# Performance work log

Measured on AMD Instinct MI355X. Metric: run time of the kernel, lower is better.

The kernel has to match this reference:

```python
import jax, jax.numpy as jnp
import numpy as np

HEADS = 12
LN_EPS = 1e-5


def setup_inputs() -> dict:
    B, S, D = 2, 2048, 768
    k = jax.random.key(0)
    ks = jax.random.split(k, 16)
    std = 0.02
    inp = {
        "key": jax.random.normal(ks[0], (B, S, D), jnp.float32),
        "query": jax.random.normal(ks[1], (B, S, D), jnp.float32),
        "value": jax.random.normal(ks[2], (B, S, D), jnp.float32),
        "mask": jax.random.randint(ks[3], (B, S, S), 0, 2).astype(bool),
        "Wk_w": jax.random.normal(ks[4], (D, D), jnp.float32) * std,
        "Wk_b": jnp.zeros((D,), jnp.float32),
        "Wq_w": jax.random.normal(ks[5], (D, D), jnp.float32) * std,
        "Wq_b": jnp.zeros((D,), jnp.float32),
        "Wv_w": jax.random.normal(ks[6], (D, D), jnp.float32) * std,
        "Wv_b": jnp.zeros((D,), jnp.float32),
        "Wc_w": jax.random.normal(ks[7], (D, D), jnp.float32) * std,
        "Wc_b": jnp.zeros((D,), jnp.float32),
        "ln_g": jnp.ones((D,), jnp.float32),
        "ln_b": jnp.zeros((D,), jnp.float32),
    }
    return inp


def _mha(key, query, value, mask, Wk_w, Wk_b, Wq_w, Wq_b, Wv_w, Wv_b,
         Wc_w, Wc_b, ln_g, ln_b):
    B, Sq, D = query.shape
    Sk = key.shape[1]
    H = HEADS
    hd = D // H
    scaler = np.float32(D ** 0.5)  # NOTE: source scales by sqrt(hidden_size), not sqrt(head_dim)

    # QKV projections (torch Linear: x @ W.T + b)
    hk = (key @ Wk_w.T + Wk_b).reshape(B, Sk, H, hd).transpose(2, 0, 1, 3)    # (H,B,Sk,hd)
    hq = (query @ Wq_w.T + Wq_b).reshape(B, Sq, H, hd).transpose(2, 0, 1, 3)  # (H,B,Sq,hd)
    hv = (value @ Wv_w.T + Wv_b).reshape(B, Sk, H, hd).transpose(2, 0, 1, 3)  # (H,B,Sk,hd)

    qk = jnp.einsum('hbqd,hbkd->hbqk', hq, hk) / scaler
    qk = jnp.where(mask[None], -jnp.inf, qk)  # mask repeated over heads in source
    attn = jax.nn.softmax(qk, axis=-1)        # dropout is identity in eval
    out = jnp.einsum('hbqk,hbkd->hbqd', attn, hv)  # (H,B,Sq,hd)

    # Faithful replication of source reshape chain:
    # (H*B,Sq,hd).view(B,H,Sq,hd).permute(1,2,0,3).view(B,Sq,D)
    out = out.reshape(B, H, Sq, hd)             # flat reinterpretation, head-major data
    out = jnp.transpose(out, (1, 2, 0, 3)).reshape(B, Sq, D)

    out = out @ Wc_w.T + Wc_b                   # Wconcat; dropout identity
    x = out + query                             # residual
    mu = jnp.mean(x, axis=-1, keepdims=True)
    var = jnp.mean((x - mu) ** 2, axis=-1, keepdims=True)
    return ln_g * (x - mu) / jnp.sqrt(var + LN_EPS) + ln_b


def reference(key, query, value, mask, Wk_w, Wk_b, Wq_w, Wq_b, Wv_w, Wv_b,
              Wc_w, Wc_b, ln_g, ln_b):
    return _mha(key, query, value, mask, Wk_w, Wk_b, Wq_w, Wq_b,
                Wv_w, Wv_b, Wc_w, Wc_b, ln_g, ln_b)
```

## Files before the change

kernel.cpp:

```cpp
#include <hip/hip_runtime.h>
#include <stdint.h>

typedef float v4f __attribute__((ext_vector_type(4)));
typedef short v8s __attribute__((ext_vector_type(8)));

#define AS1 __attribute__((address_space(1)))
#define AS3 __attribute__((address_space(3)))

__device__ __forceinline__ void load16_to_lds(const void* g, void* l) {
  __builtin_amdgcn_global_load_lds((AS1 void*)g, (AS3 void*)l, 16, 0, 0);
}
__device__ __forceinline__ void load4_to_lds(const void* g, void* l) {
  __builtin_amdgcn_global_load_lds((AS1 void*)g, (AS3 void*)l, 4, 0, 0);
}

__device__ __forceinline__ float fexp2(float x) {
#if __has_builtin(__builtin_amdgcn_exp2f)
  return __builtin_amdgcn_exp2f(x);
#else
  return exp2f(x);
#endif
}

__device__ __forceinline__ unsigned short f2bf_rn(float f) {
  union { float f; uint32_t u; } v; v.f = f;
  return (unsigned short)((v.u + 0x8000u) >> 16);
}
__device__ __forceinline__ uint32_t pack_bf2(float x, float y) {
  union { float f; uint32_t u; } a, b; a.f = x; b.f = y;
  return __builtin_amdgcn_perm(b.u + 0x8000u, a.u + 0x8000u, 0x07060302u);
}

#define QSCALE 0.052058786f

__global__ __launch_bounds__(256) void pack_mask_kernel(
    const uint32_t* __restrict__ mask, uint32_t* __restrict__ bits) {
  __shared__ int s_i32;
  const int tid = threadIdx.x;
  if (tid == 0) s_i32 = 1;
  __syncthreads();
  if (mask[tid] > 1u) s_i32 = 0;
  __syncthreads();
  if (s_i32) {
    const int lane = tid & 63;
    const int gw = (blockIdx.x * 256 + tid) >> 6;
#pragma unroll 4
    for (int it = 0; it < 32; ++it) {
      const size_t base = (size_t)gw * 2048 + it * 64;
      unsigned long long bal = __ballot(mask[base + lane] != 0u);
      if (lane == 0) *(unsigned long long*)&bits[base >> 5] = bal;
    }
  } else {
    const int wi = blockIdx.x * 256 + tid;
    const uint32_t* p = mask + (size_t)wi * 8;
    uint32_t w = 0;
#pragma unroll
    for (int j8 = 0; j8 < 8; ++j8) {
      uint32_t u = p[j8];
#pragma unroll
      for (int k = 0; k < 4; ++k)
        w |= (((u >> (8 * k)) & 0xFFu) ? 1u : 0u) << (j8 * 4 + k);
    }
    bits[wi] = w;
  }
}

__global__ __launch_bounds__(256) void conv_kernel(
    const float* __restrict__ wk, const float* __restrict__ wq,
    const float* __restrict__ wv, const float* __restrict__ wc,
    const float* __restrict__ kin, const float* __restrict__ qin,
    const float* __restrict__ vin,
    unsigned short* __restrict__ dk, unsigned short* __restrict__ dq,
    unsigned short* __restrict__ dv, unsigned short* __restrict__ dc,
    unsigned short* __restrict__ dki, unsigned short* __restrict__ dqi,
    unsigned short* __restrict__ dvi) {
  const int y = blockIdx.y;
  const float* s; unsigned short* d; float sc = 1.f; int n4;
  switch (y) {
    case 0: s = wk;  d = dk;  n4 = 147456; break;
    case 1: s = wq;  d = dq;  n4 = 147456; sc = QSCALE; break;
    case 2: s = wv;  d = dv;  n4 = 147456; break;
    case 3: s = wc;  d = dc;  n4 = 147456; break;
    case 4: s = kin; d = dki; n4 = 786432; break;
    case 5: s = qin; d = dqi; n4 = 786432; break;
    default: s = vin; d = dvi; n4 = 786432; break;
  }
  const int i = blockIdx.x * 256 + threadIdx.x;
  if (i >= n4) return;
  float4 f = ((const float4*)s)[i];
  uint2 o;
  o.x = pack_bf2(f.x * sc, f.y * sc);
  o.y = pack_bf2(f.z * sc, f.w * sc);
  ((uint2*)d)[i] = o;
}

__global__ __launch_bounds__(256, 3) void gemm_qkv_kernel(
    const unsigned short* __restrict__ qin, const unsigned short* __restrict__ kin,
    const unsigned short* __restrict__ vin,
    const unsigned short* __restrict__ wqb, const unsigned short* __restrict__ wkb,
    const unsigned short* __restrict__ wvb,
    const float* __restrict__ bq, const float* __restrict__ bk,
    const float* __restrict__ bv,
    unsigned short* __restrict__ Qb, unsigned short* __restrict__ Kb,
    unsigned short* __restrict__ Vt) {
  const int which = blockIdx.z;
  const unsigned short* A; const unsigned short* Wb; const float* bias;
  float bscale = 1.f;
  if (which == 0)      { A = qin; Wb = wqb; bias = bq; bscale = QSCALE; }
  else if (which == 1) { A = kin; Wb = wkb; bias = bk; }
  else                 { A = vin; Wb = wvb; bias = bv; }

  const int m0 = blockIdx.x * 128, n0 = blockIdx.y * 128;
  const int tid = threadIdx.x, lane = tid & 63, wid = tid >> 6;
  const int wm = wid >> 1, wn = wid & 1;
  const int l16 = lane & 15, quad = lane >> 4;

  __shared__ __align__(16) unsigned short As[2][128 * 32];
  __shared__ __align__(16) unsigned short Bs[2][128 * 32];

  v4f acc[4][4];
#pragma unroll
  for (int i = 0; i < 4; ++i)
#pragma unroll
    for (int j = 0; j < 4; ++j) { v4f z = {0.f, 0.f, 0.f, 0.f}; acc[i][j] = z; }

  const int c0 = wid * 128 + lane, c1 = wid * 128 + 64 + lane;
  const unsigned short* a0 = A + (size_t)(m0 + (c0 >> 2)) * 768 + (c0 & 3) * 8;
  const unsigned short* a1 = A + (size_t)(m0 + (c1 >> 2)) * 768 + (c1 & 3) * 8;
  const unsigned short* b0 = Wb + (size_t)(n0 + (c0 >> 2)) * 768 + (c0 & 3) * 8;
  const unsigned short* b1 = Wb + (size_t)(n0 + (c1 >> 2)) * 768 + (c1 & 3) * 8;

#define QKV_STAGE(k0, buf)                                         \
  do {                                                             \
    load16_to_lds(a0 + (k0), &As[buf][(wid * 128) * 8]);           \
    load16_to_lds(a1 + (k0), &As[buf][(wid * 128 + 64) * 8]);      \
    load16_to_lds(b0 + (k0), &Bs[buf][(wid * 128) * 8]);           \
    load16_to_lds(b1 + (k0), &Bs[buf][(wid * 128 + 64) * 8]);      \
  } while (0)

  QKV_STAGE(0, 0);
#pragma unroll 2
  for (int ks = 0; ks < 24; ++ks) {
    const int bufc = ks & 1;
    __syncthreads();
    v8s af[4], bf[4];
#pragma unroll
    for (int i = 0; i < 4; ++i)
      af[i] = *(const v8s*)&As[bufc][(wm * 64 + i * 16 + l16) * 32 + quad * 8];
#pragma unroll
    for (int j = 0; j < 4; ++j)
      bf[j] = *(const v8s*)&Bs[bufc][(wn * 64 + j * 16 + l16) * 32 + quad * 8];
    if (ks < 23) QKV_STAGE((ks + 1) * 32, bufc ^ 1);
#pragma unroll
    for (int i = 0; i < 4; ++i)
#pragma unroll
      for (int j = 0; j < 4; ++j)
        acc[i][j] = __builtin_amdgcn_mfma_f32_16x16x32_bf16(af[i], bf[j],
                                                            acc[i][j], 0, 0, 0);
  }
#undef QKV_STAGE

#pragma unroll
  for (int i = 0; i < 4; ++i) {
#pragma unroll
    for (int j = 0; j < 4; ++j) {
      const int mbase = m0 + wm * 64 + i * 16 + quad * 4;
      const int n = n0 + wn * 64 + j * 16 + l16;
      const float bv_ = bias[n] * bscale;
      if (which == 2) {
        const int bb = mbase >> 11, ss = mbase & 2047;
        uint2 pk;
        pk.x = pack_bf2(acc[i][j][0] + bv_, acc[i][j][1] + bv_);
        pk.y = pack_bf2(acc[i][j][2] + bv_, acc[i][j][3] + bv_);
        *(uint2*)&Vt[((size_t)bb * 768 + n) * 2048 + ss] = pk;
      } else {
        unsigned short* dst = (which == 0) ? Qb : Kb;
#pragma unroll
        for (int r = 0; r < 4; ++r)
          dst[(size_t)(mbase + r) * 768 + n] = f2bf_rn(acc[i][j][r] + bv_);
      }
    }
  }
}

__global__ __launch_bounds__(256, 3) void attn_kernel(
    const unsigned short* __restrict__ Qb, const unsigned short* __restrict__ Kb,
    const unsigned short* __restrict__ Vt, const uint32_t* __restrict__ mbits,
    unsigned short* __restrict__ X) {
  const int q0 = blockIdx.x * 64;
  const int h = blockIdx.y, b = blockIdx.z;
  const int tid = threadIdx.x, w = tid >> 6, lane = tid & 63;
  const int l16 = lane & 15, quad = lane >> 4, l7 = l16 & 7;

  __shared__ __align__(16) unsigned short Kl[2][64 * 64];
  __shared__ __align__(16) unsigned short Vl[2][64 * 64];
  __shared__ __align__(16) unsigned short Pl[4][16 * 64];
  __shared__ uint32_t Ml[2][128];

  v8s aq[2];
  {
    const unsigned short* qp =
        Qb + (size_t)(b * 2048 + q0 + w * 16 + l16) * 768 + h * 64 + quad * 8;
    aq[0] = *(const v8s*)qp;
    aq[1] = *(const v8s*)(qp + 32);
  }

  v4f o[4], ol;
#pragma unroll
  for (int nt = 0; nt < 4; ++nt) { v4f z = {0.f, 0.f, 0.f, 0.f}; o[nt] = z; }
  { v4f z = {0.f, 0.f, 0.f, 0.f}; ol = z; }

  v8s bones;
  {
    const short v1 = (l16 == 0) ? (short)0x3F80 : (short)0;
#pragma unroll
    for (int j = 0; j < 8; ++j) bones[j] = v1;
  }

  const int rsub = lane >> 3;
  const int csub = ((lane & 7) ^ rsub) * 8;
  const unsigned short* kg0 = Kb + (size_t)(b * 2048 + w * 16) * 768 + h * 64;
  const unsigned short* vg0 = Vt + (size_t)(b * 768 + h * 64 + w * 16) * 2048;
  const uint32_t* mg0 =
      mbits + (size_t)(b * 2048 + q0 + w * 32 + (lane >> 1)) * 64 + (lane & 1);

#define ATTN_STAGE(kk0, buf)                                                  \
  do {                                                                        \
    const unsigned short* kg = kg0 + (size_t)(kk0) * 768;                     \
    const unsigned short* vg = vg0 + (kk0);                                   \
    load16_to_lds(kg + (size_t)rsub * 768 + csub, &Kl[buf][(w * 16) * 64]);   \
    load16_to_lds(kg + (size_t)(8 + rsub) * 768 + csub,                       \
                  &Kl[buf][(w * 16 + 8) * 64]);                               \
    load16_to_lds(vg + (size_t)rsub * 2048 + csub, &Vl[buf][(w * 16) * 64]);  \
    load16_to_lds(vg + (size_t)(8 + rsub) * 2048 + csub,                      \
                  &Vl[buf][(w * 16 + 8) * 64]);                               \
    if (w < 2) load4_to_lds(mg0 + ((kk0) >> 5), &Ml[buf][w * 64]);            \
  } while (0)

  ATTN_STAGE(0, 0);
#pragma unroll 2
  for (int it = 0; it < 32; ++it) {
    const int bufc = it & 1;
    __syncthreads();

    v8s bk[2][4];
#pragma unroll
    for (int kt = 0; kt < 2; ++kt)
#pragma unroll
      for (int nt = 0; nt < 4; ++nt)
        bk[kt][nt] = *(const v8s*)&Kl[bufc][(nt * 16 + l16) * 64 +
                                           (((kt * 4 + quad) ^ l7) << 3)];
    if (it < 31) ATTN_STAGE((it + 1) * 64, bufc ^ 1);

    v4f sacc[4];
#pragma unroll
    for (int nt = 0; nt < 4; ++nt) { v4f z = {0.f, 0.f, 0.f, 0.f}; sacc[nt] = z; }
#pragma unroll
    for (int kt = 0; kt < 2; ++kt)
#pragma unroll
      for (int nt = 0; nt < 4; ++nt)
        sacc[nt] = __builtin_amdgcn_mfma_f32_16x16x32_bf16(aq[kt], bk[kt][nt],
                                                           sacc[nt], 0, 0, 0);

    const int rowb = w * 16 + quad * 4;
    const int hi = l16 >> 3;
#pragma unroll
    for (int r = 0; r < 4; ++r) {
      const uint2 mw = *(const uint2*)&Ml[bufc][(rowb + r - w * 16 + w * 16) * 2];
      const uint32_t u0 = mw.x >> l16, u1 = mw.y >> l16;
      const float p0 = (u0 & 1u) ? 0.f : fexp2(sacc[0][r]);
      const float p1 = ((u0 >> 16) & 1u) ? 0.f : fexp2(sacc[1][r]);
      const float p2 = (u1 & 1u) ? 0.f : fexp2(sacc[2][r]);
      const float p3 = ((u1 >> 16) & 1u) ? 0.f : fexp2(sacc[3][r]);
      const int prow = quad * 4 + r, ps = prow & 7;
      const int base = prow * 64 + l7;
      Pl[w][base + (((0 + hi) ^ ps) << 3)] = f2bf_rn(p0);
      Pl[w][base + (((2 + hi) ^ ps) << 3)] = f2bf_rn(p1);
      Pl[w][base + (((4 + hi) ^ ps) << 3)] = f2bf_rn(p2);
      Pl[w][base + (((6 + hi) ^ ps) << 3)] = f2bf_rn(p3);
    }

#pragma unroll
    for (int kt = 0; kt < 2; ++kt) {
      const v8s ap = *(const v8s*)&Pl[w][l16 * 64 + (((kt * 4 + quad) ^ l7) << 3)];
#pragma unroll
      for (int nt = 0; nt < 4; ++nt) {
        const v8s bv = *(const v8s*)&Vl[bufc][(nt * 16 + l16) * 64 +
                                             (((kt * 4 + quad) ^ l7) << 3)];
        o[nt] = __builtin_amdgcn_mfma_f32_16x16x32_bf16(ap, bv, o[nt], 0, 0, 0);
      }
      ol = __builtin_amdgcn_mfma_f32_16x16x32_bf16(ap, bones, ol, 0, 0, 0);
    }
  }
#undef ATTN_STAGE

  const int hb2 = 2 * h + b;
  const int b2 = (hb2 >= 12) ? 1 : 0;
  const int h2 = hb2 - 12 * b2;
#pragma unroll
  for (int r = 0; r < 4; ++r) {
    const float lsum = __shfl(ol[r], quad * 16, 64);
    const float inv_l = 1.f / lsum;
    const int q = q0 + w * 16 + quad * 4 + r;
#pragma unroll
    for (int nt = 0; nt < 4; ++nt) {
      const int d = nt * 16 + l16;
      const size_t f = (size_t)h2 * 262144 + (size_t)q * 128 + b2 * 64 + d;
      X[f] = f2bf_rn(o[nt][r] * inv_l);
    }
  }
}

__global__ __launch_bounds__(256, 3) void gemm2_kernel(
    const unsigned short* __restrict__ X, const unsigned short* __restrict__ Wcb,
    const float* __restrict__ bc, const float* __restrict__ query,
    float* __restrict__ out) {
  const int m0 = blockIdx.x * 64, n0 = blockIdx.y * 128;
  const int tid = threadIdx.x, lane = tid & 63, wid = tid >> 6;
  const int wm = wid >> 1, wn = wid & 1;
  const int l16 = lane & 15, quad = lane >> 4;

  __shared__ __align__(16) unsigned short As[2][64 * 32];
  __shared__ __align__(16) unsigned short Bs[2][128 * 32];

  v4f acc[2][4];
#pragma unroll
  for (int i = 0; i < 2; ++i)
#pragma unroll
    for (int j = 0; j < 4; ++j) { v4f z = {0.f, 0.f, 0.f, 0.f}; acc[i][j] = z; }

  const int ca = tid;
  const unsigned short* a0 = X + (size_t)(m0 + (ca >> 2)) * 768 + (ca & 3) * 8;
  const int c0 = wid * 128 + lane, c1 = wid * 128 + 64 + lane;
  const unsigned short* b0 = Wcb + (size_t)(n0 + (c0 >> 2)) * 768 + (c0 & 3) * 8;
  const unsigned short* b1 = Wcb + (size_t)(n0 + (c1 >> 2)) * 768 + (c1 & 3) * 8;

#define G2_STAGE(k0, buf)                                        \
  do {                                                           \
    load16_to_lds(a0 + (k0), &As[buf][(wid * 64) * 8]);          \
    load16_to_lds(b0 + (k0), &Bs[buf][(wid * 128) * 8]);         \
    load16_to_lds(b1 + (k0), &Bs[buf][(wid * 128 + 64) * 8]);    \
  } while (0)

  G2_STAGE(0, 0);
#pragma unroll 2
  for (int ks = 0; ks < 24; ++ks) {
    const int bufc = ks & 1;
    __syncthreads();
    v8s af[2], bf[4];
#pragma unroll
    for (int i = 0; i < 2; ++i)
      af[i] = *(const v8s*)&As[bufc][(wm * 32 + i * 16 + l16) * 32 + quad * 8];
#pragma unroll
    for (int j = 0; j < 4; ++j)
      bf[j] = *(const v8s*)&Bs[bufc][(wn * 64 + j * 16 + l16) * 32 + quad * 8];
    if (ks < 23) G2_STAGE((ks + 1) * 32, bufc ^ 1);
#pragma unroll
    for (int i = 0; i < 2; ++i)
#pragma unroll
      for (int j = 0; j < 4; ++j)
        acc[i][j] = __builtin_amdgcn_mfma_f32_16x16x32_bf16(af[i], bf[j],
                                                            acc[i][j], 0, 0, 0);
  }
#undef G2_STAGE

#pragma unroll
  for (int i = 0; i < 2; ++i) {
#pragma unroll
    for (int j = 0; j < 4; ++j) {
      const int mbase = m0 + wm * 32 + i * 16 + quad * 4;
      const int n = n0 + wn * 64 + j * 16 + l16;
      const float bv_ = bc[n];
#pragma unroll
      for (int r = 0; r < 4; ++r) {
        const int m = mbase + r;
        out[(size_t)m * 768 + n] =
            acc[i][j][r] + bv_ + query[(size_t)m * 768 + n];
      }
    }
  }
}

__global__ __launch_bounds__(256) void ln_kernel(float* __restrict__ out,
                                                 const float* __restrict__ g,
                                                 const float* __restrict__ bta) {
  const int row = blockIdx.x;
  const int tid = threadIdx.x;
  float x[3];
  float s = 0.f, sq = 0.f;
#pragma unroll
  for (int k = 0; k < 3; ++k) {
    x[k] = out[(size_t)row * 768 + tid + k * 256];
    s += x[k];
    sq += x[k] * x[k];
  }
#pragma unroll
  for (int off = 1; off < 64; off <<= 1) {
    s += __shfl_xor(s, off, 64);
    sq += __shfl_xor(sq, off, 64);
  }
  __shared__ float ss[4], ssq[4];
  const int w = tid >> 6, lane = tid & 63;
  if (lane == 0) { ss[w] = s; ssq[w] = sq; }
  __syncthreads();
  s = ss[0] + ss[1] + ss[2] + ss[3];
  sq = ssq[0] + ssq[1] + ssq[2] + ssq[3];
  const float mu = s * (1.f / 768.f);
  const float var = sq * (1.f / 768.f) - mu * mu;
  const float rstd = rsqrtf(var + 1e-5f);
#pragma unroll
  for (int k = 0; k < 3; ++k) {
    const int cc = tid + k * 256;
    out[(size_t)row * 768 + cc] = g[cc] * (x[k] - mu) * rstd + bta[cc];
  }
}

extern "C" void kernel_launch(void* const* d_in, const int* in_sizes, int n_in,
                              void* d_out, int out_size, void* d_ws,
                              size_t ws_size, hipStream_t stream) {
  const float* key   = (const float*)d_in[0];
  const float* query = (const float*)d_in[1];
  const float* value = (const float*)d_in[2];
  const uint32_t* mask = (const uint32_t*)d_in[3];
  const float* Wk = (const float*)d_in[4];
  const float* bk = (const float*)d_in[5];
  const float* Wq = (const float*)d_in[6];
  const float* bq = (const float*)d_in[7];
  const float* Wv = (const float*)d_in[8];
  const float* bv = (const float*)d_in[9];
  const float* Wc = (const float*)d_in[10];
  const float* bc = (const float*)d_in[11];
  const float* lng = (const float*)d_in[12];
  const float* lnb = (const float*)d_in[13];

  char* ws = (char*)d_ws;
  uint32_t*       mbits = (uint32_t*)(ws);
  unsigned short* Wkb = (unsigned short*)(ws + 0x100000);
  unsigned short* Wqb = (unsigned short*)(ws + 0x220000);
  unsigned short* Wvb = (unsigned short*)(ws + 0x340000);
  unsigned short* Wcb = (unsigned short*)(ws + 0x460000);
  unsigned short* Qb  = (unsigned short*)(ws + 0x600000);
  unsigned short* Kb  = (unsigned short*)(ws + 0xC00000);
  unsigned short* Vt  = (unsigned short*)(ws + 0x1200000);
  unsigned short* X   = (unsigned short*)(ws + 0x1800000);
  unsigned short* Kin = (unsigned short*)d_out;
  unsigned short* Qin = (unsigned short*)d_out + 3145728;
  unsigned short* Vin = X;
  float* out = (float*)d_out;

  pack_mask_kernel<<<dim3(1024), dim3(256), 0, stream>>>(mask, mbits);
  conv_kernel<<<dim3(3072, 7), dim3(256), 0, stream>>>(
      Wk, Wq, Wv, Wc, key, query, value,
      Wkb, Wqb, Wvb, Wcb, Kin, Qin, Vin);
  gemm_qkv_kernel<<<dim3(32, 6, 3), dim3(256), 0, stream>>>(
      Qin, Kin, Vin, Wqb, Wkb, Wvb, bq, bk, bv, Qb, Kb, Vt);
  attn_kernel<<<dim3(32, 12, 2), dim3(256), 0, stream>>>(Qb, Kb, Vt, mbits, X);
  gemm2_kernel<<<dim3(64, 6), dim3(256), 0, stream>>>(X, Wcb, bc, query, out);
  ln_kernel<<<dim3(4096), dim3(256), 0, stream>>>(out, lng, lnb);
}
```

Before: 243.9 us.

## Fuse mask packing into conversion, split attention keys across waves, fuse GEMM2 with LayerNorm

Result: slower. 264.1 us (+8.3%).

```diff
diff --git a/kernel.cpp b/kernel.cpp
--- a/kernel.cpp
+++ b/kernel.cpp
@@ -33,48 +33,48 @@
 
 #define QSCALE 0.052058786f
 
-__global__ __launch_bounds__(256) void pack_mask_kernel(
-    const uint32_t* __restrict__ mask, uint32_t* __restrict__ bits) {
-  __shared__ int s_i32;
-  const int tid = threadIdx.x;
-  if (tid == 0) s_i32 = 1;
-  __syncthreads();
-  if (mask[tid] > 1u) s_i32 = 0;
-  __syncthreads();
-  if (s_i32) {
-    const int lane = tid & 63;
-    const int gw = (blockIdx.x * 256 + tid) >> 6;
-#pragma unroll 4
-    for (int it = 0; it < 32; ++it) {
-      const size_t base = (size_t)gw * 2048 + it * 64;
-      unsigned long long bal = __ballot(mask[base + lane] != 0u);
-      if (lane == 0) *(unsigned long long*)&bits[base >> 5] = bal;
-    }
-  } else {
-    const int wi = blockIdx.x * 256 + tid;
-    const uint32_t* p = mask + (size_t)wi * 8;
-    uint32_t w = 0;
-#pragma unroll
-    for (int j8 = 0; j8 < 8; ++j8) {
-      uint32_t u = p[j8];
-#pragma unroll
-      for (int k = 0; k < 4; ++k)
-        w |= (((u >> (8 * k)) & 0xFFu) ? 1u : 0u) << (j8 * 4 + k);
-    }
-    bits[wi] = w;
-  }
-}
-
-__global__ __launch_bounds__(256) void conv_kernel(
+__global__ __launch_bounds__(256) void conv_pack_kernel(
     const float* __restrict__ wk, const float* __restrict__ wq,
     const float* __restrict__ wv, const float* __restrict__ wc,
     const float* __restrict__ kin, const float* __restrict__ qin,
-    const float* __restrict__ vin,
+    const float* __restrict__ vin, const uint32_t* __restrict__ mask,
     unsigned short* __restrict__ dk, unsigned short* __restrict__ dq,
     unsigned short* __restrict__ dv, unsigned short* __restrict__ dc,
     unsigned short* __restrict__ dki, unsigned short* __restrict__ dqi,
-    unsigned short* __restrict__ dvi) {
+    unsigned short* __restrict__ dvi, uint32_t* __restrict__ bits) {
   const int y = blockIdx.y;
+  const int tid = threadIdx.x;
+  if (y == 7) {
+    if (blockIdx.x >= 1024) return;
+    __shared__ int s_i32;
+    if (tid == 0) s_i32 = 1;
+    __syncthreads();
+    if (mask[tid] > 1u) s_i32 = 0;
+    __syncthreads();
+    if (s_i32) {
+      const int lane = tid & 63;
+      const int gw = (blockIdx.x * 256 + tid) >> 6;
+#pragma unroll 4
+      for (int it = 0; it < 32; ++it) {
+        const size_t base = (size_t)gw * 2048 + it * 64;
+        unsigned long long bal = __ballot(mask[base + lane] != 0u);
+        if (lane == 0) *(unsigned long long*)&bits[base >> 5] = bal;
+      }
+    } else {
+      const int wi = blockIdx.x * 256 + tid;
+      const uint32_t* p = mask + (size_t)wi * 8;
+      uint32_t w = 0;
+#pragma unroll
+      for (int j8 = 0; j8 < 8; ++j8) {
+        uint32_t u = p[j8];
+#pragma unroll
+        for (int k = 0; k < 4; ++k)
+          w |= (((u >> (8 * k)) & 0xFFu) ? 1u : 0u) << (j8 * 4 + k);
+      }
+      bits[wi] = w;
+    }
+    return;
+  }
   const float* s; unsigned short* d; float sc = 1.f; int n4;
   switch (y) {
     case 0: s = wk;  d = dk;  n4 = 147456; break;
@@ -85,7 +85,7 @@
     case 5: s = qin; d = dqi; n4 = 786432; break;
     default: s = vin; d = dvi; n4 = 786432; break;
   }
-  const int i = blockIdx.x * 256 + threadIdx.x;
+  const int i = blockIdx.x * 256 + tid;
   if (i >= n4) return;
   float4 f = ((const float4*)s)[i];
   uint2 o;
@@ -191,24 +191,32 @@
   const int h = blockIdx.y, b = blockIdx.z;
   const int tid = threadIdx.x, w = tid >> 6, lane = tid & 63;
   const int l16 = lane & 15, quad = lane >> 4, l7 = l16 & 7;
-
-  __shared__ __align__(16) unsigned short Kl[2][64 * 64];
-  __shared__ __align__(16) unsigned short Vl[2][64 * 64];
-  __shared__ __align__(16) unsigned short Pl[4][16 * 64];
-  __shared__ uint32_t Ml[2][128];
-
-  v8s aq[2];
-  {
+  const int wq = w >> 1, wk = w & 1;
+
+  __shared__ __align__(16) char smem[41984];
+  unsigned short* Kl = (unsigned short*)smem;
+  unsigned short* Vl = (unsigned short*)(smem + 16384);
+  unsigned short* Pl = (unsigned short*)(smem + 32768);
+  uint32_t*       Ml = (uint32_t*)(smem + 40960);
+  float*          sc = (float*)smem;
+
+  v8s aq[2][2];
+#pragma unroll
+  for (int mi = 0; mi < 2; ++mi) {
     const unsigned short* qp =
-        Qb + (size_t)(b * 2048 + q0 + w * 16 + l16) * 768 + h * 64 + quad * 8;
-    aq[0] = *(const v8s*)qp;
-    aq[1] = *(const v8s*)(qp + 32);
-  }
-
-  v4f o[4], ol;
-#pragma unroll
-  for (int nt = 0; nt < 4; ++nt) { v4f z = {0.f, 0.f, 0.f, 0.f}; o[nt] = z; }
-  { v4f z = {0.f, 0.f, 0.f, 0.f}; ol = z; }
+        Qb + (size_t)(b * 2048 + q0 + wq * 32 + mi * 16 + l16) * 768 + h * 64 +
+        quad * 8;
+    aq[mi][0] = *(const v8s*)qp;
+    aq[mi][1] = *(const v8s*)(qp + 32);
+  }
+
+  v4f o[2][4], ol[2];
+#pragma unroll
+  for (int mi = 0; mi < 2; ++mi) {
+#pragma unroll
+    for (int nt = 0; nt < 4; ++nt) { v4f z = {0.f, 0.f, 0.f, 0.f}; o[mi][nt] = z; }
+    v4f z = {0.f, 0.f, 0.f, 0.f}; ol[mi] = z;
+  }
 
   v8s bones;
   {
@@ -224,17 +232,19 @@
   const uint32_t* mg0 =
       mbits + (size_t)(b * 2048 + q0 + w * 32 + (lane >> 1)) * 64 + (lane & 1);
 
-#define ATTN_STAGE(kk0, buf)                                                  \
-  do {                                                                        \
-    const unsigned short* kg = kg0 + (size_t)(kk0) * 768;                     \
-    const unsigned short* vg = vg0 + (kk0);                                   \
-    load16_to_lds(kg + (size_t)rsub * 768 + csub, &Kl[buf][(w * 16) * 64]);   \
-    load16_to_lds(kg + (size_t)(8 + rsub) * 768 + csub,                       \
-                  &Kl[buf][(w * 16 + 8) * 64]);                               \
-    load16_to_lds(vg + (size_t)rsub * 2048 + csub, &Vl[buf][(w * 16) * 64]);  \
-    load16_to_lds(vg + (size_t)(8 + rsub) * 2048 + csub,                      \
-                  &Vl[buf][(w * 16 + 8) * 64]);                               \
-    if (w < 2) load4_to_lds(mg0 + ((kk0) >> 5), &Ml[buf][w * 64]);            \
+#define ATTN_STAGE(kk0, buf)                                                   \
+  do {                                                                         \
+    const unsigned short* kg = kg0 + (size_t)(kk0) * 768;                      \
+    const unsigned short* vg = vg0 + (kk0);                                    \
+    load16_to_lds(kg + (size_t)rsub * 768 + csub,                              \
+                  &Kl[(buf) * 4096 + (w * 16) * 64]);                          \
+    load16_to_lds(kg + (size_t)(8 + rsub) * 768 + csub,                        \
+                  &Kl[(buf) * 4096 + (w * 16 + 8) * 64]);                      \
+    load16_to_lds(vg + (size_t)rsub * 2048 + csub,                             \
+                  &Vl[(buf) * 4096 + (w * 16) * 64]);                          \
+    load16_to_lds(vg + (size_t)(8 + rsub) * 2048 + csub,                       \
+                  &Vl[(buf) * 4096 + (w * 16 + 8) * 64]);                      \
+    if (w < 2) load4_to_lds(mg0 + ((kk0) >> 5), &Ml[(buf) * 128 + w * 64]);    \
   } while (0)
 
   ATTN_STAGE(0, 0);
@@ -243,103 +253,135 @@
     const int bufc = it & 1;
     __syncthreads();
 
-    v8s bk[2][4];
+    v8s bk[2][2];
+#pragma unroll
+    for (int ni = 0; ni < 2; ++ni)
+#pragma unroll
+      for (int kt = 0; kt < 2; ++kt)
+        bk[ni][kt] = *(const v8s*)&Kl[bufc * 4096 +
+                                      (wk * 32 + ni * 16 + l16) * 64 +
+                                      (((kt * 4 + quad) ^ l7) << 3)];
+    if (it < 31) ATTN_STAGE((it + 1) * 64, bufc ^ 1);
+
+    v4f sacc[2][2];
+#pragma unroll
+    for (int mi = 0; mi < 2; ++mi)
+#pragma unroll
+      for (int ni = 0; ni < 2; ++ni) {
+        v4f z = {0.f, 0.f, 0.f, 0.f};
+        sacc[mi][ni] = z;
+      }
 #pragma unroll
     for (int kt = 0; kt < 2; ++kt)
 #pragma unroll
+      for (int mi = 0; mi < 2; ++mi)
+#pragma unroll
+        for (int ni = 0; ni < 2; ++ni)
+          sacc[mi][ni] = __builtin_amdgcn_mfma_f32_16x16x32_bf16(
+              aq[mi][kt], bk[ni][kt], sacc[mi][ni], 0, 0, 0);
+
+    const int hi = l16 >> 3;
+#pragma unroll
+    for (int mi = 0; mi < 2; ++mi) {
+#pragma unroll
+      for (int r = 0; r < 4; ++r) {
+        const int row = wq * 32 + mi * 16 + quad * 4 + r;
+        const uint32_t u = Ml[bufc * 128 + row * 2 + wk] >> l16;
+        const float p0 = (u & 1u) ? 0.f : fexp2(sacc[mi][0][r]);
+        const float p1 = ((u >> 16) & 1u) ? 0.f : fexp2(sacc[mi][1][r]);
+        const int ps = (quad * 4 + r) & 7;
+        const int base = row * 64 + l7;
+        Pl[base + (((wk * 4 + 0 + hi) ^ ps) << 3)] = f2bf_rn(p0);
+        Pl[base + (((wk * 4 + 2 + hi) ^ ps) << 3)] = f2bf_rn(p1);
+      }
+    }
+
+#pragma unroll
+    for (int mi = 0; mi < 2; ++mi) {
+      const v8s ap = *(const v8s*)&Pl[(wq * 32 + mi * 16 + l16) * 64 +
+                                      (((wk * 4 + quad) ^ l7) << 3)];
+#pragma unroll
+      for (int nt = 0; nt < 4; ++nt) {
+        const v8s bv = *(const v8s*)&Vl[bufc * 4096 + (nt * 16 + l16) * 64 +
+                                        (((wk * 4 + quad) ^ l7) << 3)];
+        o[mi][nt] =
+            __builtin_amdgcn_mfma_f32_16x16x32_bf16(ap, bv, o[mi][nt], 0, 0, 0);
+      }
+      ol[mi] = __builtin_amdgcn_mfma_f32_16x16x32_bf16(ap, bones, ol[mi], 0, 0, 0);
+    }
+  }
+#undef ATTN_STAGE
+
+  __syncthreads();
+  const int sbase = (wq * 64 + lane) * 44;
+  if (wk) {
+#pragma unroll
+    for (int mi = 0; mi < 2; ++mi)
+#pragma unroll
       for (int nt = 0; nt < 4; ++nt)
-        bk[kt][nt] = *(const v8s*)&Kl[bufc][(nt * 16 + l16) * 64 +
-                                           (((kt * 4 + quad) ^ l7) << 3)];
-    if (it < 31) ATTN_STAGE((it + 1) * 64, bufc ^ 1);
-
-    v4f sacc[4];
-#pragma unroll
-    for (int nt = 0; nt < 4; ++nt) { v4f z = {0.f, 0.f, 0.f, 0.f}; sacc[nt] = z; }
-#pragma unroll
-    for (int kt = 0; kt < 2; ++kt)
+        *(v4f*)&sc[sbase + (mi * 4 + nt) * 4] = o[mi][nt];
+    *(v4f*)&sc[sbase + 32] = ol[0];
+    *(v4f*)&sc[sbase + 36] = ol[1];
+  }
+  __syncthreads();
+  if (!wk) {
+#pragma unroll
+    for (int mi = 0; mi < 2; ++mi)
 #pragma unroll
       for (int nt = 0; nt < 4; ++nt)
-        sacc[nt] = __builtin_amdgcn_mfma_f32_16x16x32_bf16(aq[kt], bk[kt][nt],
-                                                           sacc[nt], 0, 0, 0);
-
-    const int rowb = w * 16 + quad * 4;
-    const int hi = l16 >> 3;
-#pragma unroll
-    for (int r = 0; r < 4; ++r) {
-      const uint2 mw = *(const uint2*)&Ml[bufc][(rowb + r - w * 16 + w * 16) * 2];
-      const uint32_t u0 = mw.x >> l16, u1 = mw.y >> l16;
-      const float p0 = (u0 & 1u) ? 0.f : fexp2(sacc[0][r]);
-      const float p1 = ((u0 >> 16) & 1u) ? 0.f : fexp2(sacc[1][r]);
-      const float p2 = (u1 & 1u) ? 0.f : fexp2(sacc[2][r]);
-      const float p3 = ((u1 >> 16) & 1u) ? 0.f : fexp2(sacc[3][r]);
-      const int prow = quad * 4 + r, ps = prow & 7;
-      const int base = prow * 64 + l7;
-      Pl[w][base + (((0 + hi) ^ ps) << 3)] = f2bf_rn(p0);
-      Pl[w][base + (((2 + hi) ^ ps) << 3)] = f2bf_rn(p1);
-      Pl[w][base + (((4 + hi) ^ ps) << 3)] = f2bf_rn(p2);
-      Pl[w][base + (((6 + hi) ^ ps) << 3)] = f2bf_rn(p3);
-    }
-
-#pragma unroll
-    for (int kt = 0; kt < 2; ++kt) {
-      const v8s ap = *(const v8s*)&Pl[w][l16 * 64 + (((kt * 4 + quad) ^ l7) << 3)];
-#pragma unroll
-      for (int nt = 0; nt < 4; ++nt) {
-        const v8s bv = *(const v8s*)&Vl[bufc][(nt * 16 + l16) * 64 +
-                                             (((kt * 4 + quad) ^ l7) << 3)];
-        o[nt] = __builtin_amdgcn_mfma_f32_16x16x32_bf16(ap, bv, o[nt], 0, 0, 0);
-      }
-      ol = __builtin_amdgcn_mfma_f32_16x16x32_bf16(ap, bones, ol, 0, 0, 0);
-    }
-  }
-#undef ATTN_STAGE
-
-  const int hb2 = 2 * h + b;
-  const int b2 = (hb2 >= 12) ? 1 : 0;
-  const int h2 = hb2 - 12 * b2;
-#pragma unroll
-  for (int r = 0; r < 4; ++r) {
-    const float lsum = __shfl(ol[r], quad * 16, 64);
-    const float inv_l = 1.f / lsum;
-    const int q = q0 + w * 16 + quad * 4 + r;
-#pragma unroll
-    for (int nt = 0; nt < 4; ++nt) {
-      const int d = nt * 16 + l16;
-      const size_t f = (size_t)h2 * 262144 + (size_t)q * 128 + b2 * 64 + d;
-      X[f] = f2bf_rn(o[nt][r] * inv_l);
-    }
-  }
-}
-
-__global__ __launch_bounds__(256, 3) void gemm2_kernel(
+        o[mi][nt] += *(const v4f*)&sc[sbase + (mi * 4 + nt) * 4];
+    ol[0] += *(const v4f*)&sc[sbase + 32];
+    ol[1] += *(const v4f*)&sc[sbase + 36];
+
+    const int hb2 = 2 * h + b;
+    const int b2 = (hb2 >= 12) ? 1 : 0;
+    const int h2 = hb2 - 12 * b2;
+#pragma unroll
+    for (int mi = 0; mi < 2; ++mi) {
+#pragma unroll
+      for (int r = 0; r < 4; ++r) {
+        const float lsum = __shfl(ol[mi][r], quad * 16, 64);
+        const float inv_l = 1.f / lsum;
+        const int q = q0 + wq * 32 + mi * 16 + quad * 4 + r;
+#pragma unroll
+        for (int nt = 0; nt < 4; ++nt) {
+          const int d = nt * 16 + l16;
+          const size_t f = (size_t)h2 * 262144 + (size_t)q * 128 + b2 * 64 + d;
+          X[f] = f2bf_rn(o[mi][nt][r] * inv_l);
+        }
+      }
+    }
+  }
+}
+
+__global__ __launch_bounds__(256, 1) void gemm2ln_kernel(
     const unsigned short* __restrict__ X, const unsigned short* __restrict__ Wcb,
     const float* __restrict__ bc, const float* __restrict__ query,
+    const float* __restrict__ lng, const float* __restrict__ lnb,
     float* __restrict__ out) {
-  const int m0 = blockIdx.x * 64, n0 = blockIdx.y * 128;
+  const int m0 = blockIdx.x * 16;
   const int tid = threadIdx.x, lane = tid & 63, wid = tid >> 6;
-  const int wm = wid >> 1, wn = wid & 1;
   const int l16 = lane & 15, quad = lane >> 4;
 
-  __shared__ __align__(16) unsigned short As[2][64 * 32];
-  __shared__ __align__(16) unsigned short Bs[2][128 * 32];
-
-  v4f acc[2][4];
-#pragma unroll
-  for (int i = 0; i < 2; ++i)
-#pragma unroll
-    for (int j = 0; j < 4; ++j) { v4f z = {0.f, 0.f, 0.f, 0.f}; acc[i][j] = z; }
-
-  const int ca = tid;
-  const unsigned short* a0 = X + (size_t)(m0 + (ca >> 2)) * 768 + (ca & 3) * 8;
-  const int c0 = wid * 128 + lane, c1 = wid * 128 + 64 + lane;
-  const unsigned short* b0 = Wcb + (size_t)(n0 + (c0 >> 2)) * 768 + (c0 & 3) * 8;
-  const unsigned short* b1 = Wcb + (size_t)(n0 + (c1 >> 2)) * 768 + (c1 & 3) * 8;
-
-#define G2_STAGE(k0, buf)                                        \
-  do {                                                           \
-    load16_to_lds(a0 + (k0), &As[buf][(wid * 64) * 8]);          \
-    load16_to_lds(b0 + (k0), &Bs[buf][(wid * 128) * 8]);         \
-    load16_to_lds(b1 + (k0), &Bs[buf][(wid * 128 + 64) * 8]);    \
+  __shared__ __align__(16) unsigned short Bs[2][768 * 32];
+  __shared__ __align__(16) unsigned short As[2][16 * 32];
+  __shared__ float red_s[4][16], red_sq[4][16];
+
+  v4f acc[12];
+#pragma unroll
+  for (int j = 0; j < 12; ++j) { v4f z = {0.f, 0.f, 0.f, 0.f}; acc[j] = z; }
+
+  const unsigned short* a0 =
+      X + (size_t)(m0 + (lane >> 2)) * 768 + (lane & 3) * 8;
+
+#define G2_STAGE(k0, buf)                                                     \
+  do {                                                                        \
+    if (wid == 0) load16_to_lds(a0 + (k0), &As[buf][0]);                      \
+    _Pragma("unroll") for (int i = 0; i < 12; ++i) {                          \
+      const int c = wid * 768 + i * 64 + lane;                                \
+      load16_to_lds(Wcb + (size_t)(c >> 2) * 768 + (k0) + (c & 3) * 8,        \
+                    &Bs[buf][(wid * 768 + i * 64) * 8]);                      \
+    }                                                                         \
   } while (0)
 
   G2_STAGE(0, 0);
@@ -347,71 +389,62 @@
   for (int ks = 0; ks < 24; ++ks) {
     const int bufc = ks & 1;
     __syncthreads();
-    v8s af[2], bf[4];
-#pragma unroll
-    for (int i = 0; i < 2; ++i)
-      af[i] = *(const v8s*)&As[bufc][(wm * 32 + i * 16 + l16) * 32 + quad * 8];
-#pragma unroll
-    for (int j = 0; j < 4; ++j)
-      bf[j] = *(const v8s*)&Bs[bufc][(wn * 64 + j * 16 + l16) * 32 + quad * 8];
+    const v8s af = *(const v8s*)&As[bufc][l16 * 32 + quad * 8];
+    v8s bf[12];
+#pragma unroll
+    for (int j = 0; j < 12; ++j)
+      bf[j] = *(const v8s*)&Bs[bufc][(wid * 192 + j * 16 + l16) * 32 + quad * 8];
     if (ks < 23) G2_STAGE((ks + 1) * 32, bufc ^ 1);
 #pragma unroll
-    for (int i = 0; i < 2; ++i)
-#pragma unroll
-      for (int j = 0; j < 4; ++j)
-        acc[i][j] = __builtin_amdgcn_mfma_f32_16x16x32_bf16(af[i], bf[j],
-                                                            acc[i][j], 0, 0, 0);
+    for (int j = 0; j < 12; ++j)
+      acc[j] = __builtin_amdgcn_mfma_f32_16x16x32_bf16(af, bf[j], acc[j], 0, 0, 0);
   }
 #undef G2_STAGE
 
-#pragma unroll
-  for (int i = 0; i < 2; ++i) {
-#pragma unroll
-    for (int j = 0; j < 4; ++j) {
-      const int mbase = m0 + wm * 32 + i * 16 + quad * 4;
-      const int n = n0 + wn * 64 + j * 16 + l16;
-      const float bv_ = bc[n];
-#pragma unroll
-      for (int r = 0; r < 4; ++r) {
-        const int m = mbase + r;
-        out[(size_t)m * 768 + n] =
-            acc[i][j][r] + bv_ + query[(size_t)m * 768 + n];
-      }
-    }
-  }
-}
-
-__global__ __launch_bounds__(256) void ln_kernel(float* __restrict__ out,
-                                                 const float* __restrict__ g,
-                                                 const float* __restrict__ bta) {
-  const int row = blockIdx.x;
-  const int tid = threadIdx.x;
-  float x[3];
-  float s = 0.f, sq = 0.f;
-#pragma unroll
-  for (int k = 0; k < 3; ++k) {
-    x[k] = out[(size_t)row * 768 + tid + k * 256];
-    s += x[k];
-    sq += x[k] * x[k];
-  }
-#pragma unroll
-  for (int off = 1; off < 64; off <<= 1) {
-    s += __shfl_xor(s, off, 64);
-    sq += __shfl_xor(sq, off, 64);
-  }
-  __shared__ float ss[4], ssq[4];
-  const int w = tid >> 6, lane = tid & 63;
-  if (lane == 0) { ss[w] = s; ssq[w] = sq; }
+  float s[4] = {0.f, 0.f, 0.f, 0.f}, sq[4] = {0.f, 0.f, 0.f, 0.f};
+#pragma unroll
+  for (int j = 0; j < 12; ++j) {
+    const int n = wid * 192 + j * 16 + l16;
+    const float bv_ = bc[n];
+#pragma unroll
+    for (int r = 0; r < 4; ++r) {
+      const int m = m0 + quad * 4 + r;
+      const float x = acc[j][r] + bv_ + query[(size_t)m * 768 + n];
+      acc[j][r] = x;
+      s[r] += x;
+      sq[r] += x * x;
+    }
+  }
+#pragma unroll
+  for (int off = 1; off < 16; off <<= 1) {
+#pragma unroll
+    for (int r = 0; r < 4; ++r) {
+      s[r] += __shfl_xor(s[r], off, 64);
+      sq[r] += __shfl_xor(sq[r], off, 64);
+    }
+  }
+  if (l16 == 0) {
+#pragma unroll
+    for (int r = 0; r < 4; ++r) {
+      red_s[wid][quad * 4 + r] = s[r];
+      red_sq[wid][quad * 4 + r] = sq[r];
+    }
+  }
   __syncthreads();
-  s = ss[0] + ss[1] + ss[2] + ss[3];
-  sq = ssq[0] + ssq[1] + ssq[2] + ssq[3];
-  const float mu = s * (1.f / 768.f);
-  const float var = sq * (1.f / 768.f) - mu * mu;
-  const float rstd = rsqrtf(var + 1e-5f);
-#pragma unroll
-  for (int k = 0; k < 3; ++k) {
-    const int cc = tid + k * 256;
-    out[(size_t)row * 768 + cc] = g[cc] * (x[k] - mu) * rstd + bta[cc];
+#pragma unroll
+  for (int r = 0; r < 4; ++r) {
+    const int row = quad * 4 + r;
+    const float ts = red_s[0][row] + red_s[1][row] + red_s[2][row] + red_s[3][row];
+    const float tq = red_sq[0][row] + red_sq[1][row] + red_sq[2][row] + red_sq[3][row];
+    const float mu = ts * (1.f / 768.f);
+    const float var = tq * (1.f / 768.f) - mu * mu;
+    const float rstd = rsqrtf(var + 1e-5f);
+#pragma unroll
+    for (int j = 0; j < 12; ++j) {
+      const int n = wid * 192 + j * 16 + l16;
+      out[(size_t)(m0 + row) * 768 + n] =
+          lng[n] * (acc[j][r] - mu) * rstd + lnb[n];
+    }
   }
 }
 
@@ -448,13 +481,12 @@
   unsigned short* Vin = X;
   float* out = (float*)d_out;
 
-  pack_mask_kernel<<<dim3(1024), dim3(256), 0, stream>>>(mask, mbits);
-  conv_kernel<<<dim3(3072, 7), dim3(256), 0, stream>>>(
-      Wk, Wq, Wv, Wc, key, query, value,
-      Wkb, Wqb, Wvb, Wcb, Kin, Qin, Vin);
+  conv_pack_kernel<<<dim3(3072, 8), dim3(256), 0, stream>>>(
+      Wk, Wq, Wv, Wc, key, query, value, mask,
+      Wkb, Wqb, Wvb, Wcb, Kin, Qin, Vin, mbits);
   gemm_qkv_kernel<<<dim3(32, 6, 3), dim3(256), 0, stream>>>(
       Qin, Kin, Vin, Wqb, Wkb, Wvb, bq, bk, bv, Qb, Kb, Vt);
   attn_kernel<<<dim3(32, 12, 2), dim3(256), 0, stream>>>(Qb, Kb, Vt, mbits, X);
-  gemm2_kernel<<<dim3(64, 6), dim3(256), 0, stream>>>(X, Wcb, bc, query, out);
-  ln_kernel<<<dim3(4096), dim3(256), 0, stream>>>(out, lng, lnb);
-}
+  gemm2ln_kernel<<<dim3(256), dim3(256), 0, stream>>>(X, Wcb, bc, query, lng,
+                                                      lnb, out);
+}
```
